# Kernel tuning notes

Measured on AMD Instinct MI355X. Metric: run time of the kernel, lower is better.

## Reference

```python
import jax, jax.numpy as jnp
import numpy as np

HID = 128          # args.hidden_dim
B = 8              # batch_size
N = 256            # num_nodes per graph (uniform)
L = 48             # num_colours / levels per graph (uniform, logk=False)
CELLS = B * N * L  # 98304 'cell' nodes
E = 250000         # edges per edge type
STEPS = 2          # args.msg_passing_steps


def setup_inputs() -> dict:
    key = jax.random.key(0)
    ks = jax.random.split(key, 20)
    s = 0.05
    d = {}
    d["q"] = jax.random.randint(ks[0], (CELLS,), 0, 3)
    d["edge_src"] = jax.random.randint(ks[1], (2, E), 0, CELLS)
    d["edge_dst"] = jax.random.randint(ks[2], (2, E), 0, CELLS)
    d["embed"] = jax.random.normal(ks[3], (3, HID), jnp.float32) * s
    # per-edge-type 4-layer MLP (stacked along axis 0: [intra, inter])
    d["msg_W0"] = jax.random.normal(ks[4], (2, HID, 2 * HID), jnp.float32) * s
    d["msg_b0"] = jnp.zeros((2, HID), jnp.float32)
    d["msg_W1"] = jax.random.normal(ks[5], (2, HID, HID), jnp.float32) * s
    d["msg_b1"] = jnp.zeros((2, HID), jnp.float32)
    d["msg_W2"] = jax.random.normal(ks[6], (2, HID, HID), jnp.float32) * s
    d["msg_b2"] = jnp.zeros((2, HID), jnp.float32)
    d["msg_W3"] = jax.random.normal(ks[7], (2, HID, HID), jnp.float32) * s
    d["msg_b3"] = jnp.zeros((2, HID), jnp.float32)
    # LSTMCell, bias=False: input = cat(x, m_intra, m_inter) -> 3*HID
    d["lstm_Wih"] = jax.random.normal(ks[8], (4 * HID, 3 * HID), jnp.float32) * s
    d["lstm_Whh"] = jax.random.normal(ks[9], (4 * HID, HID), jnp.float32) * s
    d["score_w"] = jax.random.normal(ks[10], (1, HID), jnp.float32) * s
    return d


def reference(q, edge_src, edge_dst, embed, msg_W0, msg_b0, msg_W1, msg_b1,
              msg_W2, msg_b2, msg_W3, msg_b3, lstm_Wih, lstm_Whh, score_w):
    x = embed[q]  # [CELLS, HID]

    def edge_msgs(h):
        msgs = []
        for et in range(2):  # structural loop over the 2 edge types
            src, dst = edge_src[et], edge_dst[et]
            m = jnp.concatenate([h[src], h[dst]], axis=-1)  # [E, 2H]
            m = jax.nn.relu(m @ msg_W0[et].T + msg_b0[et])
            m = jax.nn.relu(m @ msg_W1[et].T + msg_b1[et])
            m = jax.nn.relu(m @ msg_W2[et].T + msg_b2[et])
            m = m @ msg_W3[et].T + msg_b3[et]
            msgs.append(jax.ops.segment_sum(m, dst, num_segments=CELLS))
        return msgs

    def step(carry, _):
        h, rh, rc = carry
        m_intra, m_inter = edge_msgs(h)
        lstm_in = jnp.concatenate([x, m_intra, m_inter], axis=-1)  # [CELLS, 3H]
        gates = lstm_in @ lstm_Wih.T + rh @ lstm_Whh.T              # [CELLS, 4H]
        i, f, g, o = jnp.split(gates, 4, axis=-1)
        nc = jax.nn.sigmoid(f) * rc + jax.nn.sigmoid(i) * jnp.tanh(g)
        nh = jax.nn.sigmoid(o) * jnp.tanh(nc)
        return (nh, nh, nc), nh

    zeros = jnp.zeros_like(x)
    _, outs = jax.lax.scan(step, (x, zeros, zeros), None, length=STEPS)
    # outs: [STEPS, CELLS, HID]; uniform sizes make get_padded_tensor a reshape:
    # [STEPS, B, L, N, HID] -> score -> view(STEPS, B*N*L)
    logits = (outs @ score_w[0]).reshape(STEPS, B * L * N)
    return logits
```

## Files before the change

kernel.cpp:

```cpp
#include <hip/hip_runtime.h>

#define HID 128
#define CELLS 98304
#define NE 250000
#define NSTEPS 2
#define NWIN 3912

typedef __attribute__((ext_vector_type(8))) short short8;
typedef __attribute__((ext_vector_type(4))) float f32x4;
typedef unsigned short u16;

__device__ __forceinline__ int permf(int s) { return ((s & 7) << 4) | (s >> 3); }
__device__ __forceinline__ int nat_of_pos(int p) {
  int l = p & 63, hf = p >> 6;
  int slot = ((l >> 2) << 3) + (hf << 2) + (l & 3);
  return ((slot & 7) << 4) | (slot >> 3);
}

__device__ __forceinline__ u16 f2bf(float f) {
  unsigned int u = __builtin_bit_cast(unsigned int, f);
  u += 0x7fffu + ((u >> 16) & 1u);
  return (u16)(u >> 16);
}
__device__ __forceinline__ float bf2f(u16 s) {
  unsigned int u = ((unsigned int)s) << 16;
  return __builtin_bit_cast(float, u);
}
__device__ __forceinline__ float sigm(float x) { return 1.f / (1.f + __expf(-x)); }
__device__ __forceinline__ float tanha(float x) { return 1.f - 2.f / (__expf(2.f * x) + 1.f); }

__device__ __forceinline__ void gload_lds16(const u16* g, u16* l) {
  __builtin_amdgcn_global_load_lds(
      (const __attribute__((address_space(1))) unsigned int*)(const void*)g,
      (__attribute__((address_space(3))) unsigned int*)(void*)l, 16, 0, 0);
}

__device__ __forceinline__ void stage_w(const u16* __restrict__ ws, u16* wl, int w, int lane) {
  #pragma unroll
  for (int i = 0; i < 2; ++i)
    gload_lds16(ws + i * 4096 + w * 512 + lane * 8, wl + i * 4096 + w * 512);
}

__global__ void prep_kernel(
    const float* __restrict__ W0, const float* __restrict__ W1,
    const float* __restrict__ W2, const float* __restrict__ W3,
    const float* __restrict__ b0, const float* __restrict__ b1,
    const float* __restrict__ b2, const float* __restrict__ b3,
    const float* __restrict__ Wih, const float* __restrict__ Whh,
    const float* __restrict__ embed, const float* __restrict__ sw,
    u16* __restrict__ W0b, u16* __restrict__ W123b,
    u16* __restrict__ Wcb, float* __restrict__ bp,
    u16* __restrict__ embp, float* __restrict__ swp)
{
  int idx = blockIdx.x * 256 + threadIdx.x;
  if (idx < 65536) {
    int et = idx >> 15, t = (idx >> 13) & 3, n = (idx >> 6) & 127, s = idx & 63;
    int g = s >> 3, j = s & 7;
    int gn = g ^ (n & 7);
    W0b[idx] = f2bf(W0[(et * 128 + n) * 256 + t * 64 + gn * 8 + j]);
    return;
  }
  idx -= 65536;
  if (idx < 98304) {
    int which = idx >> 15, r = idx & 32767;
    int et = r >> 14, hh = (r >> 13) & 1, n = (r >> 6) & 127, s = r & 63;
    int g = s >> 3, j = s & 7;
    int gn = g ^ (n & 7);
    const float* W = which == 0 ? W1 : (which == 1 ? W2 : W3);
    W123b[which * 32768 + r] = f2bf(W[(et * 128 + n) * 128 + permf(hh * 64 + gn * 8 + j)]);
    return;
  }
  idx -= 98304;
  if (idx < 262144) {
    int s = idx & 511, n = idx >> 9;
    int blk = s >> 7, s7 = s & 127;
    int k7 = (blk == 1 || blk == 2) ? nat_of_pos(s7) : s7;
    float v = (blk < 3) ? Wih[n * 384 + blk * 128 + k7] : Whh[n * 128 + k7];
    Wcb[idx] = f2bf(v);
    return;
  }
  idx -= 262144;
  if (idx < 1024) {
    int l = idx >> 8, r = idx & 255;
    int et = r >> 7, s = r & 127;
    const float* b = l == 0 ? b0 : (l == 1 ? b1 : (l == 2 ? b2 : b3));
    bp[idx] = b[et * 128 + permf(s)];
    return;
  }
  idx -= 1024;
  if (idx < 384) {
    embp[idx] = f2bf(embed[idx]);
    return;
  }
  idx -= 384;
  if (idx < 128) swp[idx] = sw[idx];
}

__global__ void init_kernel(const int* __restrict__ q, const u16* __restrict__ embp,
                            u16* __restrict__ xb, u16* __restrict__ h)
{
  int idx = blockIdx.x * 256 + threadIdx.x;
  int c = idx >> 7, s = idx & 127;
  u16 v = embp[q[c] * 128 + s];
  xb[idx] = v;
  h[idx] = v;
}

__global__ void hist_kernel(const int* __restrict__ edst, int* __restrict__ counts)
{
  int idx = blockIdx.x * 256 + threadIdx.x;
  if (idx >= 2 * NE) return;
  int et = (idx >= NE) ? 1 : 0;
  atomicAdd(&counts[et * CELLS + edst[idx]], 1);
}

__global__ void scan1_kernel(const int* __restrict__ counts, int* __restrict__ S,
                             int* __restrict__ btot)
{
  __shared__ int sh[1024];
  const int t = threadIdx.x, b = blockIdx.x;
  const int i = b * 1024 + t;
  int v = counts[i];
  sh[t] = v;
  __syncthreads();
  int acc = v;
  for (int off = 1; off < 1024; off <<= 1) {
    int add = (t >= off) ? sh[t - off] : 0;
    __syncthreads();
    acc += add;
    sh[t] = acc;
    __syncthreads();
  }
  S[i] = acc - v;
  if (t == 1023) btot[b] = acc;
}

__global__ void scan2_kernel(const int* __restrict__ btot, int* __restrict__ boffs,
                             int* __restrict__ S)
{
  __shared__ int sh[256];
  const int t = threadIdx.x;
  int v = (t < 192) ? btot[t] : 0;
  sh[t] = v;
  __syncthreads();
  int acc = v;
  for (int off = 1; off < 256; off <<= 1) {
    int add = (t >= off) ? sh[t - off] : 0;
    __syncthreads();
    acc += add;
    sh[t] = acc;
    __syncthreads();
  }
  if (t < 192) boffs[t] = acc - v;
  if (t == 0) S[2 * CELLS] = 2 * NE;
}

__global__ void scan3_kernel(int* __restrict__ S, const int* __restrict__ boffs)
{
  const int i = blockIdx.x * 1024 + threadIdx.x;
  S[i] += boffs[blockIdx.x];
}

__global__ void scatter_kernel(const int* __restrict__ esrc, const int* __restrict__ edst,
                               const int* __restrict__ S, int* __restrict__ fill,
                               int* __restrict__ ssrc, int* __restrict__ sdst)
{
  int idx = blockIdx.x * 256 + threadIdx.x;
  if (idx >= 2 * NE) return;
  int et = (idx >= NE) ? 1 : 0;
  int d = edst[idx];
  int pos = atomicAdd(&fill[et * CELLS + d], 1);
  int slot = S[et * CELLS + d] - et * NE + pos;
  sdst[et * NE + slot] = d;
  ssrc[et * NE + slot] = esrc[idx];
}

__device__ __forceinline__ void bias_relu_store(f32x4 (&acc)[4][8], const float* __restrict__ bl,
                                                u16* __restrict__ ab, int q, int c)
{
  float bias[8];
  #pragma unroll
  for (int j = 0; j < 8; ++j) bias[j] = bl[c * 8 + j];
  #pragma unroll
  for (int mt = 0; mt < 4; ++mt) {
    #pragma unroll
    for (int r = 0; r < 4; ++r) {
      const int rowl = mt * 16 + 4 * q + r;
      short8 t;
      #pragma unroll
      for (int nt = 0; nt < 8; ++nt) {
        float v = acc[mt][nt][r] + bias[nt];
        v = v > 0.f ? v : 0.f;
        t[nt] = (short)f2bf(v);
      }
      *(short8*)(ab + rowl * 128 + ((c ^ (rowl & 15)) << 3)) = t;
    }
  }
}

__launch_bounds__(512, 2)
__global__ void msg_kernel(
    const u16* __restrict__ h,
    const int* __restrict__ ssrc, const int* __restrict__ sdst,
    const int* __restrict__ S,
    const u16* __restrict__ W0b, const u16* __restrict__ W123b,
    const float* __restrict__ bp,
    u16* __restrict__ m0, u16* __restrict__ m1,
    int* __restrict__ side_dst, float* __restrict__ side_part)
{
  __shared__ u16 abuf[8][64 * 128];
  __shared__ u16 wbuf[64 * 128];
  const int et = blockIdx.y;
  const int tid = threadIdx.x;
  const int w = tid >> 6, lane = tid & 63, q = lane >> 4, c = lane & 15;
  const int ebase = blockIdx.x * 512 + w * 64;
  const int win = blockIdx.x * 8 + w;
  const int* __restrict__ src = ssrc + et * NE;
  const int* __restrict__ dst = sdst + et * NE;
  u16* __restrict__ msgs = (et == 0) ? m0 : m1;
  u16* ab = abuf[w];

  int eS = ebase + lane;
  if (eS >= NE) eS = NE - 1;
  const int srow = src[eS];

  int rowD[4];
  #pragma unroll
  for (int mt = 0; mt < 4; ++mt) {
    int e = ebase + mt * 16 + c;
    if (e >= NE) e = NE - 1;
    rowD[mt] = dst[e];
  }

  #pragma unroll
  for (int i = 0; i < 16; ++i) {
    const int r = i * 4 + (lane >> 4);
    const int grow = __shfl(srow, r);
    const int cg = lane & 15;
    gload_lds16(h + (size_t)grow * 128 + ((cg ^ (r & 15)) << 3), ab + i * 512);
  }
  stage_w(W0b + (et * 4 + 2) * 8192, wbuf, w, lane);

  const int eL = ebase + lane;
  const int dval = (eL < NE) ? dst[eL] : -1;
  int rpS = 0, rpE = 0;
  if (dval >= 0) {
    rpS = S[et * CELLS + dval] - et * NE;
    rpE = S[et * CELLS + dval + 1] - et * NE;
  }
  const int dlagged = __shfl_up(dval, 1);
  const bool headp = (lane == 0) | (dval != dlagged);
  const unsigned long long tails = (__ballot(headp) >> 1) | (1ull << 63);
  const unsigned long long intmask = __ballot(dval >= 0 && rpS >= ebase && rpE <= ebase + 64);

  const f32x4 zf = {0.f, 0.f, 0.f, 0.f};
  f32x4 acc[4][8];
  #pragma unroll
  for (int mt = 0; mt < 4; ++mt)
    #pragma unroll
    for (int nt = 0; nt < 8; ++nt) acc[mt][nt] = zf;

  asm volatile("s_waitcnt vmcnt(0)" ::: "memory");
  __syncthreads();

  #pragma unroll 1
  for (int t = 2; t < 4; ++t) {
    if (t == 3) {
      __syncthreads();
      stage_w(W0b + (et * 4 + 3) * 8192, wbuf, w, lane);
      asm volatile("s_waitcnt vmcnt(0)" ::: "memory");
      __syncthreads();
    }
    #pragma unroll
    for (int ks = 0; ks < 2; ++ks) {
      const int kqh = (t - 2) * 64 + ks * 32 + q * 8;
      short8 a[4], b[8];
      #pragma unroll
      for (int mt = 0; mt < 4; ++mt)
        a[mt] = *(const short8*)(h + (size_t)rowD[mt] * HID + kqh);
      #pragma unroll
      for (int nt = 0; nt < 8; ++nt)
        b[nt] = *(const short8*)(wbuf + (nt * 16 + c) * 64 + (((ks * 4 + q) ^ (c & 7)) << 3));
      #pragma unroll
      for (int mt = 0; mt < 4; ++mt)
        #pragma unroll
        for (int nt = 0; nt < 8; ++nt)
          acc[mt][nt] = __builtin_amdgcn_mfma_f32_16x16x32_bf16(a[mt], b[nt], acc[mt][nt], 0, 0, 0);
    }
  }

  #pragma unroll 1
  for (int t = 0; t < 2; ++t) {
    __syncthreads();
    stage_w(W0b + (et * 4 + t) * 8192, wbuf, w, lane);
    asm volatile("s_waitcnt vmcnt(0)" ::: "memory");
    __syncthreads();
    #pragma unroll
    for (int ks = 0; ks < 2; ++ks) {
      const int blk = t * 8 + ks * 4 + q;
      short8 a[4], b[8];
      #pragma unroll
      for (int mt = 0; mt < 4; ++mt) {
        const int row = mt * 16 + c;
        a[mt] = *(const short8*)(ab + row * 128 + ((blk ^ c) << 3));
      }
      #pragma unroll
      for (int nt = 0; nt < 8; ++nt)
        b[nt] = *(const short8*)(wbuf + (nt * 16 + c) * 64 + (((ks * 4 + q) ^ (c & 7)) << 3));
      #pragma unroll
      for (int mt = 0; mt < 4; ++mt)
        #pragma unroll
        for (int nt = 0; nt < 8; ++nt)
          acc[mt][nt] = __builtin_amdgcn_mfma_f32_16x16x32_bf16(a[mt], b[nt], acc[mt][nt], 0, 0, 0);
    }
  }

  #pragma unroll 1
  for (int l = 1; l <= 3; ++l) {
    #pragma unroll 1
    for (int hh = 0; hh < 2; ++hh) {
      __syncthreads();
      stage_w(W123b + (((l - 1) * 2 + et) * 2 + hh) * 8192, wbuf, w, lane);
      if (hh == 0) bias_relu_store(acc, bp + (l - 1) * 256 + et * 128, ab, q, c);
      asm volatile("s_waitcnt vmcnt(0)" ::: "memory");
      __syncthreads();
      if (hh == 0) {
        #pragma unroll
        for (int mt = 0; mt < 4; ++mt)
          #pragma unroll
          for (int nt = 0; nt < 8; ++nt) acc[mt][nt] = zf;
      }
      #pragma unroll
      for (int ks = 0; ks < 2; ++ks) {
        const int blk = hh * 8 + ks * 4 + q;
        short8 a[4], b[8];
        #pragma unroll
        for (int mt = 0; mt < 4; ++mt) {
          const int row = mt * 16 + c;
          a[mt] = *(const short8*)(ab + row * 128 + ((blk ^ c) << 3));
        }
        #pragma unroll
        for (int nt = 0; nt < 8; ++nt)
          b[nt] = *(const short8*)(wbuf + (nt * 16 + c) * 64 + (((ks * 4 + q) ^ (c & 7)) << 3));
        #pragma unroll
        for (int mt = 0; mt < 4; ++mt)
          #pragma unroll
          for (int nt = 0; nt < 8; ++nt)
            acc[mt][nt] = __builtin_amdgcn_mfma_f32_16x16x32_bf16(a[mt], b[nt], acc[mt][nt], 0, 0, 0);
      }
    }
  }

  float bias[8];
  #pragma unroll
  for (int j = 0; j < 8; ++j) bias[j] = bp[3 * 256 + et * 128 + c * 8 + j];

  float* fab = (float*)ab;
  #pragma unroll
  for (int half = 0; half < 2; ++half) {
    #pragma unroll
    for (int mt = 0; mt < 4; ++mt) {
      #pragma unroll
      for (int r = 0; r < 4; ++r) {
        const int row = mt * 16 + 4 * q + r;
        f32x4 t;
        #pragma unroll
        for (int nti = 0; nti < 4; ++nti)
          t[nti] = acc[mt][half * 4 + nti][r] + bias[half * 4 + nti];
        *(f32x4*)(fab + row * 64 + c * 4) = t;
      }
    }
    float run = 0.f;
    int jstart = 0;
    #pragma unroll 1
    for (int jb = 0; jb < 64; jb += 8) {
      #pragma unroll
      for (int u = 0; u < 8; ++u) {
        const int j = jb + u;
        run += fab[j * 64 + lane];
        if ((tails >> j) & 1) {
          const int d = __builtin_amdgcn_readlane(dval, j);
          if (d >= 0) {
            if ((intmask >> j) & 1) {
              msgs[(size_t)d * HID + half * 64 + lane] = f2bf(run);
            } else {
              const int slot = (jstart == 0) ? 0 : 1;
              const size_t sb = ((size_t)et * NWIN + win) * 2 + slot;
              side_part[sb * 128 + half * 64 + lane] = run;
              if (lane == 0 && half == 0) side_dst[sb] = d;
            }
          }
          run = 0.f;
          jstart = j + 1;
        }
      }
    }
  }
}

__global__ void fixup_kernel(const int* __restrict__ S,
                             const int* __restrict__ side_dst,
                             const float* __restrict__ side_part,
                             u16* __restrict__ m0, u16* __restrict__ m1)
{
  const int b = blockIdx.x;
  const int et = b / NWIN, win = b - et * NWIN;
  const int t = threadIdx.x;
  u16* __restrict__ m = et ? m1 : m0;
  #pragma unroll
  for (int s = 0; s < 2; ++s) {
    const int d = side_dst[b * 2 + s];
    if (d < 0) continue;
    const int r0 = S[et * CELLS + d] - et * NE;
    if ((r0 >> 6) != win) continue;
    const int w1 = (S[et * CELLS + d + 1] - et * NE - 1) >> 6;
    float sum = 0.f;
    for (int wi = win; wi <= w1; ++wi) {
      const int base = (et * NWIN + wi) * 2;
      if (side_dst[base + 0] == d) sum += side_part[(size_t)(base + 0) * 128 + t];
      if (side_dst[base + 1] == d) sum += side_part[(size_t)(base + 1) * 128 + t];
    }
    m[(size_t)d * HID + t] = f2bf(sum);
  }
}

__launch_bounds__(512, 4)
__global__ void lstm_kernel(
    const int step,
    const u16* __restrict__ xb, const u16* __restrict__ mm0, const u16* __restrict__ mm1,
    u16* __restrict__ h, u16* __restrict__ rc,
    const u16* __restrict__ Wcb, const float* __restrict__ swp,
    float* __restrict__ out)
{
  __shared__ u16 at[64 * 512];
  const int tid = threadIdx.x;
  const int cb = blockIdx.x * 64;

  for (int base = tid * 8; base < 64 * 512; base += 4096) {
    const int cl = base >> 9, s = base & 511;
    const int cell = cb + cl;
    short8 t;
    if (s < 128) {
      t = *(const short8*)(xb + cell * 128 + s);
    } else if (s < 384) {
      const u16* mp = (s < 256 ? mm0 : mm1) + cell * 128 + (s & 127);
      t = *(const short8*)(mp);
    } else if (step == 0) {
      #pragma unroll
      for (int j = 0; j < 8; ++j) t[j] = 0;
    } else {
      t = *(const short8*)(h + cell * 128 + (s & 127));
    }
    const int blk = s >> 3;
    const int blks = (blk & 48) | ((blk ^ cl) & 15);
    *(short8*)(at + cl * 512 + blks * 8) = t;
  }
  __syncthreads();

  const int w = tid >> 6, lane = tid & 63, q = lane >> 4, c = lane & 15;
  const int wf = w;
  const f32x4 zf = {0.f, 0.f, 0.f, 0.f};
  f32x4 acc[4][4];
  #pragma unroll
  for (int mt = 0; mt < 4; ++mt)
    #pragma unroll
    for (int g = 0; g < 4; ++g) acc[mt][g] = zf;

  #pragma unroll
  for (int ks = 0; ks < 16; ++ks) {
    const int kq = ks * 32 + q * 8;
    const int blk = kq >> 3;
    short8 a[4], b[4];
    #pragma unroll
    for (int mt = 0; mt < 4; ++mt) {
      const int row = mt * 16 + c;
      const int blks = (blk & 48) | ((blk ^ c) & 15);
      a[mt] = *(const short8*)(at + row * 512 + blks * 8);
    }
    #pragma unroll
    for (int g = 0; g < 4; ++g)
      b[g] = *(const short8*)(Wcb + (g * 128 + wf * 16 + c) * 512 + kq);
    #pragma unroll
    for (int mt = 0; mt < 4; ++mt)
      #pragma unroll
      for (int g = 0; g < 4; ++g)
        acc[mt][g] = __builtin_amdgcn_mfma_f32_16x16x32_bf16(a[mt], b[g], acc[mt][g], 0, 0, 0);
  }
  __syncthreads();

  const float swc = swp[wf * 16 + c];
  const bool last = (step == NSTEPS - 1);
  float* pt = (float*)at;
  #pragma unroll
  for (int mt = 0; mt < 4; ++mt) {
    #pragma unroll
    for (int r = 0; r < 4; ++r) {
      const int cl = mt * 16 + 4 * q + r;
      const int cell = cb + cl;
      const float ig = sigm(acc[mt][0][r]);
      const float fg = sigm(acc[mt][1][r]);
      const float gg = tanha(acc[mt][2][r]);
      const float og = sigm(acc[mt][3][r]);
      u16* rcp = rc + (size_t)cell * HID + wf * 16 + c;
      const float c0 = (step == 0) ? 0.f : bf2f(rcp[0]);
      const float nc = fg * c0 + ig * gg;
      const float nhv = og * tanha(nc);
      if (!last) {
        rcp[0] = f2bf(nc);
        h[(size_t)cell * HID + wf * 16 + c] = f2bf(nhv);
      }
      float v = nhv * swc;
      v += __shfl_xor(v, 1); v += __shfl_xor(v, 2);
      v += __shfl_xor(v, 4); v += __shfl_xor(v, 8);
      if (c == 0) pt[wf * 64 + cl] = v;
    }
  }
  __syncthreads();
  if (tid < 64) {
    float s = 0.f;
    #pragma unroll
    for (int ww = 0; ww < 8; ++ww) s += pt[ww * 64 + tid];
    out[step * CELLS + cb + tid] = s;
  }
}

extern "C" void kernel_launch(void* const* d_in, const int* in_sizes, int n_in,
                              void* d_out, int out_size, void* d_ws, size_t ws_size,
                              hipStream_t stream)
{
  const int* q      = (const int*)d_in[0];
  const int* esrc   = (const int*)d_in[1];
  const int* edst   = (const int*)d_in[2];
  const float* embed= (const float*)d_in[3];
  const float* W0   = (const float*)d_in[4];
  const float* b0   = (const float*)d_in[5];
  const float* W1   = (const float*)d_in[6];
  const float* b1   = (const float*)d_in[7];
  const float* W2   = (const float*)d_in[8];
  const float* b2   = (const float*)d_in[9];
  const float* W3   = (const float*)d_in[10];
  const float* b3   = (const float*)d_in[11];
  const float* Wih  = (const float*)d_in[12];
  const float* Whh  = (const float*)d_in[13];
  const float* sw   = (const float*)d_in[14];

  char* ws = (char*)d_ws;
  size_t off = 0;
  auto alloc = [&](size_t bytes) {
    void* p = ws + off;
    off += (bytes + 255) & ~(size_t)255;
    return p;
  };
  u16*   h    = (u16*)  alloc((size_t)CELLS * HID * 2);
  u16*   xb   = (u16*)  alloc((size_t)CELLS * HID * 2);
  u16*   rc   = (u16*)  alloc((size_t)CELLS * HID * 2);
  u16*   m0   = (u16*)  alloc((size_t)CELLS * HID * 2);
  u16*   m1   = (u16*)  alloc((size_t)CELLS * HID * 2);
  u16*   W0b  = (u16*)  alloc(2 * 128 * 256 * 2);
  u16*   W123b= (u16*)  alloc((size_t)3 * 2 * 128 * 128 * 2);
  u16*   Wcb  = (u16*)  alloc(512 * 512 * 2);
  float* bp   = (float*)alloc(4 * 256 * 4);
  u16*   embp = (u16*)  alloc(384 * 2);
  float* swp  = (float*)alloc(128 * 4);
  int*   counts = (int*)alloc((size_t)2 * CELLS * 4);
  int*   Sarr   = (int*)alloc(((size_t)2 * CELLS + 1) * 4);
  int*   fill   = (int*)alloc((size_t)2 * CELLS * 4);
  int*   btot   = (int*)alloc(192 * 4);
  int*   boffs  = (int*)alloc(192 * 4);
  int*   ssrc   = (int*)alloc((size_t)2 * NE * 4);
  int*   sdst   = (int*)alloc((size_t)2 * NE * 4);
  int*   side_dst  = (int*)  alloc((size_t)2 * NWIN * 2 * 4);
  float* side_part = (float*)alloc((size_t)2 * NWIN * 2 * 128 * 4);

  prep_kernel<<<1670, 256, 0, stream>>>(W0, W1, W2, W3, b0, b1, b2, b3, Wih, Whh, embed, sw,
                                        W0b, W123b, Wcb, bp, embp, swp);
  init_kernel<<<(CELLS * HID) / 256, 256, 0, stream>>>(q, embp, xb, h);

  hipMemsetAsync(counts, 0, (size_t)2 * CELLS * 4, stream);
  hipMemsetAsync(fill, 0, (size_t)2 * CELLS * 4, stream);
  hist_kernel<<<(2 * NE + 255) / 256, 256, 0, stream>>>(edst, counts);
  scan1_kernel<<<192, 1024, 0, stream>>>(counts, Sarr, btot);
  scan2_kernel<<<1, 256, 0, stream>>>(btot, boffs, Sarr);
  scan3_kernel<<<192, 1024, 0, stream>>>(Sarr, boffs);
  scatter_kernel<<<(2 * NE + 255) / 256, 256, 0, stream>>>(esrc, edst, Sarr, fill, ssrc, sdst);

  hipMemsetAsync(m0, 0, (size_t)2 * CELLS * HID * 2, stream);
  hipMemsetAsync(side_dst, 0xFF, (size_t)2 * NWIN * 2 * 4, stream);

  for (int step = 0; step < NSTEPS; ++step) {
    msg_kernel<<<dim3((NE + 511) / 512, 2), 512, 0, stream>>>(h, ssrc, sdst, Sarr,
                                                              W0b, W123b, bp,
                                                              m0, m1, side_dst, side_part);
    fixup_kernel<<<2 * NWIN, 128, 0, stream>>>(Sarr, side_dst, side_part, m0, m1);
    lstm_kernel<<<CELLS / 64, 512, 0, stream>>>(step, xb, m0, m1, h, rc, Wcb, swp, (float*)d_out);
  }
}
```

Measured before the change: 748.2 us.

## Double-buffer weight tiles in LDS to overlap staging with MFMA compute

Merges the three separate weight-staging loops of the message MLP into one 10-iteration loop with two LDS weight buffers. Each iteration prefetches the next weight tile into the other buffer while running MFMAs on the current one, then syncs once. This cuts the barrier pairs and exposed global-load latency of staging each weight tile before using it. LDS footprint grows by 16KB, which may reduce occupancy headroom.

```diff
diff --git a/kernel.cpp b/kernel.cpp
--- a/kernel.cpp
+++ b/kernel.cpp
@@ -209,7 +209,7 @@
     int* __restrict__ side_dst, float* __restrict__ side_part)
 {
   __shared__ u16 abuf[8][64 * 128];
-  __shared__ u16 wbuf[64 * 128];
+  __shared__ u16 wbuf[2][128 * 64];
   const int et = blockIdx.y;
   const int tid = threadIdx.x;
   const int w = tid >> 6, lane = tid & 63, q = lane >> 4, c = lane & 15;
@@ -239,7 +239,7 @@
     const int cg = lane & 15;
     gload_lds16(h + (size_t)grow * 128 + ((cg ^ (r & 15)) << 3), ab + i * 512);
   }
-  stage_w(W0b + (et * 4 + 2) * 8192, wbuf, w, lane);
+  stage_w(W0b + (et * 4 + 2) * 8192, wbuf[0], w, lane);
 
   const int eL = ebase + lane;
   const int dval = (eL < NE) ? dst[eL] : -1;
@@ -264,91 +264,54 @@
   __syncthreads();
 
   #pragma unroll 1
-  for (int t = 2; t < 4; ++t) {
-    if (t == 3) {
-      __syncthreads();
-      stage_w(W0b + (et * 4 + 3) * 8192, wbuf, w, lane);
-      asm volatile("s_waitcnt vmcnt(0)" ::: "memory");
-      __syncthreads();
-    }
-    #pragma unroll
-    for (int ks = 0; ks < 2; ++ks) {
-      const int kqh = (t - 2) * 64 + ks * 32 + q * 8;
-      short8 a[4], b[8];
-      #pragma unroll
-      for (int mt = 0; mt < 4; ++mt)
-        a[mt] = *(const short8*)(h + (size_t)rowD[mt] * HID + kqh);
-      #pragma unroll
-      for (int nt = 0; nt < 8; ++nt)
-        b[nt] = *(const short8*)(wbuf + (nt * 16 + c) * 64 + (((ks * 4 + q) ^ (c & 7)) << 3));
+  for (int i = 0; i < 10; ++i) {
+    if (i < 9) {
+      const int j = i + 1;
+      const u16* wsrc;
+      if (j < 4) {
+        const int t = (j < 2) ? (j + 2) : (j - 2);
+        wsrc = W0b + (et * 4 + t) * 8192;
+      } else {
+        const int li = j - 4;
+        wsrc = W123b + (li >> 1) * 32768 + et * 16384 + (li & 1) * 8192;
+      }
+      stage_w(wsrc, wbuf[j & 1], w, lane);
+    }
+    if (i >= 4 && !(i & 1)) {
+      bias_relu_store(acc, bp + ((i - 4) >> 1) * 256 + et * 128, ab, q, c);
       #pragma unroll
       for (int mt = 0; mt < 4; ++mt)
         #pragma unroll
-        for (int nt = 0; nt < 8; ++nt)
-          acc[mt][nt] = __builtin_amdgcn_mfma_f32_16x16x32_bf16(a[mt], b[nt], acc[mt][nt], 0, 0, 0);
-    }
-  }
-
-  #pragma unroll 1
-  for (int t = 0; t < 2; ++t) {
-    __syncthreads();
-    stage_w(W0b + (et * 4 + t) * 8192, wbuf, w, lane);
-    asm volatile("s_waitcnt vmcnt(0)" ::: "memory");
-    __syncthreads();
+        for (int nt = 0; nt < 8; ++nt) acc[mt][nt] = zf;
+    }
+    const u16* wb = wbuf[i & 1];
     #pragma unroll
     for (int ks = 0; ks < 2; ++ks) {
-      const int blk = t * 8 + ks * 4 + q;
       short8 a[4], b[8];
-      #pragma unroll
-      for (int mt = 0; mt < 4; ++mt) {
-        const int row = mt * 16 + c;
-        a[mt] = *(const short8*)(ab + row * 128 + ((blk ^ c) << 3));
-      }
-      #pragma unroll
-      for (int nt = 0; nt < 8; ++nt)
-        b[nt] = *(const short8*)(wbuf + (nt * 16 + c) * 64 + (((ks * 4 + q) ^ (c & 7)) << 3));
-      #pragma unroll
-      for (int mt = 0; mt < 4; ++mt)
-        #pragma unroll
-        for (int nt = 0; nt < 8; ++nt)
-          acc[mt][nt] = __builtin_amdgcn_mfma_f32_16x16x32_bf16(a[mt], b[nt], acc[mt][nt], 0, 0, 0);
-    }
-  }
-
-  #pragma unroll 1
-  for (int l = 1; l <= 3; ++l) {
-    #pragma unroll 1
-    for (int hh = 0; hh < 2; ++hh) {
-      __syncthreads();
-      stage_w(W123b + (((l - 1) * 2 + et) * 2 + hh) * 8192, wbuf, w, lane);
-      if (hh == 0) bias_relu_store(acc, bp + (l - 1) * 256 + et * 128, ab, q, c);
-      asm volatile("s_waitcnt vmcnt(0)" ::: "memory");
-      __syncthreads();
-      if (hh == 0) {
+      if (i < 2) {
+        const int kqh = i * 64 + ks * 32 + q * 8;
         #pragma unroll
         for (int mt = 0; mt < 4; ++mt)
-          #pragma unroll
-          for (int nt = 0; nt < 8; ++nt) acc[mt][nt] = zf;
-      }
-      #pragma unroll
-      for (int ks = 0; ks < 2; ++ks) {
-        const int blk = hh * 8 + ks * 4 + q;
-        short8 a[4], b[8];
+          a[mt] = *(const short8*)(h + (size_t)rowD[mt] * HID + kqh);
+      } else {
+        const int blk = (i & 1) * 8 + ks * 4 + q;
         #pragma unroll
         for (int mt = 0; mt < 4; ++mt) {
           const int row = mt * 16 + c;
           a[mt] = *(const short8*)(ab + row * 128 + ((blk ^ c) << 3));
         }
+      }
+      #pragma unroll
+      for (int nt = 0; nt < 8; ++nt)
+        b[nt] = *(const short8*)(wb + (nt * 16 + c) * 64 + (((ks * 4 + q) ^ (c & 7)) << 3));
+      #pragma unroll
+      for (int mt = 0; mt < 4; ++mt)
         #pragma unroll
         for (int nt = 0; nt < 8; ++nt)
-          b[nt] = *(const short8*)(wbuf + (nt * 16 + c) * 64 + (((ks * 4 + q) ^ (c & 7)) << 3));
-        #pragma unroll
-        for (int mt = 0; mt < 4; ++mt)
-          #pragma unroll
-          for (int nt = 0; nt < 8; ++nt)
-            acc[mt][nt] = __builtin_amdgcn_mfma_f32_16x16x32_bf16(a[mt], b[nt], acc[mt][nt], 0, 0, 0);
-      }
-    }
+          acc[mt][nt] = __builtin_amdgcn_mfma_f32_16x16x32_bf16(a[mt], b[nt], acc[mt][nt], 0, 0, 0);
+    }
+    asm volatile("s_waitcnt vmcnt(0)" ::: "memory");
+    __syncthreads();
   }
 
   float bias[8];
```

New measurement: 726.2 us. -2.9%, faster.
